# Kernel tuning notes

Measured on AMD Instinct MI355X. Metric: run time of the kernel, lower is better.

The kernel has to match this reference:

```python
import jax, jax.numpy as jnp
import numpy as np

B, M, N, K = 256, 512, 256, 16


def setup_inputs() -> dict:
    key = jax.random.key(0)
    k1, k2, k3, k4 = jax.random.split(key, 4)
    x = jax.random.normal(k1, (B, M, N), dtype=jnp.float32)
    # Linear(in_features=N, out_features=1): weight [1, N], bias [1]
    w_weight = jax.random.normal(k2, (1, N), dtype=jnp.float32) * (2.0 / (N + 1)) ** 0.5
    w_bias = jnp.zeros((1,), dtype=jnp.float32)
    # v: [N, K], xavier_normal
    v = jax.random.normal(k3, (N, K), dtype=jnp.float32) * (2.0 / (N + K)) ** 0.5
    return {"x": x, "w_weight": w_weight, "w_bias": w_bias, "v": v}


def reference(x, w_weight, w_bias, v):
    # Linear term: [B, M, 1]
    l = x @ w_weight.T + w_bias  # broadcasts bias [1]
    # Pairwise interaction. Original: result[b,a,c] = x[b,a] @ (V V^T) @ x[b,c]
    # p[b,a] = 0.5 * (sum_c result[b,a,c] - result[b,a,a])
    # Efficient O(B*M*K) identity: with xv = x @ V,
    #   sum_c result[b,a,c] = xv[b,a] . sum_c xv[b,c]
    #   result[b,a,a]       = ||xv[b,a]||^2
    xv = jnp.einsum('bmn,nk->bmk', x, v)        # [B, M, K]
    sv = xv.sum(axis=1)                          # [B, K]
    row_sum = jnp.einsum('bmk,bk->bm', xv, sv)  # [B, M]
    diag = jnp.sum(xv * xv, axis=-1)             # [B, M]
    p = 0.5 * (row_sum - diag)                   # [B, M]
    return l + p[..., None]                      # [B, M, 1]
```

## Files before the change

### kernel.cpp

```cpp
#include <hip/hip_runtime.h>

#define B_ 256
#define M_ 512
#define N_ 256
#define K_ 16
#define TR 64
#define NT 4

typedef __attribute__((ext_vector_type(8))) short short8;
typedef __attribute__((ext_vector_type(4))) float f32x4;

__device__ __forceinline__ unsigned short f2bf(float f) {
    unsigned u = __builtin_bit_cast(unsigned, f);
    u += 0x7FFFu + ((u >> 16) & 1u);
    return (unsigned short)(u >> 16);
}
__device__ __forceinline__ float bf2f(unsigned short h) {
    unsigned u = ((unsigned)h) << 16;
    return __builtin_bit_cast(float, u);
}

__global__ __launch_bounds__(256) void fm_pass1(
    const float* __restrict__ x, const float* __restrict__ w,
    const float* __restrict__ bias, const float* __restrict__ v,
    float* __restrict__ xv, float* __restrict__ svpart, float* __restrict__ out)
{
    __shared__ __align__(16) unsigned char xL[2][TR * 512];
    __shared__ __align__(16) unsigned short wLb[N_];
    __shared__ __align__(16) float red[64];

    const int t   = threadIdx.x;
    const int l   = t & 63;
    const int wv  = t >> 6;
    const int blk = blockIdx.x;
    const int b   = blk >> 1;
    const int m0  = (blk & 1) * (NT * TR);
    const float bias0 = bias[0];

    if (t < 64) {
        float4 wq = *(const float4*)(w + t * 4);
        wLb[t * 4 + 0] = f2bf(wq.x); wLb[t * 4 + 1] = f2bf(wq.y);
        wLb[t * 4 + 2] = f2bf(wq.z); wLb[t * 4 + 3] = f2bf(wq.w);
    }

    short8 vB[8];
    #pragma unroll
    for (int c = 0; c < 8; ++c) {
        #pragma unroll
        for (int j = 0; j < 8; ++j) {
            float f = v[(size_t)(c * 32 + (l >> 4) * 8 + j) * K_ + (l & 15)];
            vB[c][j] = (short)f2bf(f);
        }
    }

    const float* gx = x + (size_t)(b * M_ + m0) * N_;

    const int swq = l >> 1;
    const int shf = (l & 1) * 8;

    float4 st[16];
    #pragma unroll
    for (int j = 0; j < 16; ++j)
        st[j] = *(const float4*)(gx + j * 1024 + t * 4);
    #pragma unroll
    for (int j = 0; j < 16; ++j) {
        const int row = j * 4 + wv;
        unsigned lo = (unsigned)f2bf(st[j].x) | ((unsigned)f2bf(st[j].y) << 16);
        unsigned hi = (unsigned)f2bf(st[j].z) | ((unsigned)f2bf(st[j].w) << 16);
        unsigned* d = (unsigned*)(xL[0] + row * 512 + ((swq ^ (row & 7)) << 4) + shf);
        d[0] = lo; d[1] = hi;
    }
    __syncthreads();

    f32x4 acc[NT];
    #pragma unroll
    for (int T = 0; T < NT; ++T) acc[T] = f32x4{0.f, 0.f, 0.f, 0.f};

    #pragma unroll
    for (int T = 0; T < NT; ++T) {
        const int cur = T & 1;
        if (T + 1 < NT) {
            #pragma unroll
            for (int j = 0; j < 16; ++j)
                st[j] = *(const float4*)(gx + (size_t)(T + 1) * TR * N_ + j * 1024 + t * 4);
        }

        const int arow = wv * 16 + (l & 15);
        const unsigned char* abase = xL[cur] + arow * 512;
        #pragma unroll
        for (int c = 0; c < 8; ++c) {
            short8 a = *(const short8*)(abase + (((c * 4 + (l >> 4)) ^ (arow & 7)) << 4));
            acc[T] = __builtin_amdgcn_mfma_f32_16x16x32_bf16(a, vB[c], acc[T], 0, 0, 0);
        }

        {
            const int row = t >> 2;
            const int qt  = t & 3;
            const unsigned char* rbase = xL[cur] + row * 512;
            float ls = 0.f;
            #pragma unroll
            for (int i = 0; i < 8; ++i) {
                short8 xs = *(const short8*)(rbase + ((((qt * 8 + i)) ^ (row & 7)) << 4));
                short8 ws = *(const short8*)((const unsigned char*)wLb + qt * 128 + i * 16);
                #pragma unroll
                for (int e = 0; e < 8; ++e)
                    ls += bf2f((unsigned short)xs[e]) * bf2f((unsigned short)ws[e]);
            }
            ls += __shfl_xor(ls, 1);
            ls += __shfl_xor(ls, 2);
            if (qt == 0)
                out[(size_t)b * M_ + m0 + T * TR + row] = ls + bias0;
        }

        if (T + 1 < NT) {
            #pragma unroll
            for (int j = 0; j < 16; ++j) {
                const int row = j * 4 + wv;
                unsigned lo = (unsigned)f2bf(st[j].x) | ((unsigned)f2bf(st[j].y) << 16);
                unsigned hi = (unsigned)f2bf(st[j].z) | ((unsigned)f2bf(st[j].w) << 16);
                unsigned* d = (unsigned*)(xL[cur ^ 1] + row * 512 + ((swq ^ (row & 7)) << 4) + shf);
                d[0] = lo; d[1] = hi;
            }
        }
        __syncthreads();
    }

    #pragma unroll
    for (int T = 0; T < NT; ++T) {
        const int rbase = m0 + T * TR + wv * 16 + (l >> 4) * 4;
        #pragma unroll
        for (int r = 0; r < 4; ++r)
            xv[(size_t)(b * M_ + rbase + r) * K_ + (l & 15)] = acc[T][r];
    }

    float s = 0.f;
    #pragma unroll
    for (int T = 0; T < NT; ++T)
        s += acc[T][0] + acc[T][1] + acc[T][2] + acc[T][3];
    s += __shfl_xor(s, 16);
    s += __shfl_xor(s, 32);
    if (l < 16) red[wv * 16 + l] = s;
    __syncthreads();
    if (t < 16)
        svpart[(size_t)blk * 16 + t] = red[t] + red[16 + t] + red[32 + t] + red[48 + t];
}

__global__ __launch_bounds__(256) void fm_pass2(
    const float* __restrict__ xv, const float* __restrict__ svpart,
    float* __restrict__ out)
{
    const int t = threadIdx.x;
    const int blk = blockIdx.x;
    const int b = blk >> 1;
    const int m = (blk & 1) * 256 + t;
    __shared__ __align__(16) float svL[16];
    if (t < 16)
        svL[t] = svpart[(size_t)(b * 2 + 0) * 16 + t] + svpart[(size_t)(b * 2 + 1) * 16 + t];
    __syncthreads();

    const float4* xvp = (const float4*)(xv + ((size_t)b * M_ + m) * K_);
    float4 a0 = xvp[0], a1 = xvp[1], a2 = xvp[2], a3 = xvp[3];
    const float4* s4 = (const float4*)svL;
    float4 s0 = s4[0], s1 = s4[1], s2 = s4[2], s3 = s4[3];

    float rs = a0.x * s0.x + a0.y * s0.y + a0.z * s0.z + a0.w * s0.w
             + a1.x * s1.x + a1.y * s1.y + a1.z * s1.z + a1.w * s1.w
             + a2.x * s2.x + a2.y * s2.y + a2.z * s2.z + a2.w * s2.w
             + a3.x * s3.x + a3.y * s3.y + a3.z * s3.z + a3.w * s3.w;
    float dg = a0.x * a0.x + a0.y * a0.y + a0.z * a0.z + a0.w * a0.w
             + a1.x * a1.x + a1.y * a1.y + a1.z * a1.z + a1.w * a1.w
             + a2.x * a2.x + a2.y * a2.y + a2.z * a2.z + a2.w * a2.w
             + a3.x * a3.x + a3.y * a3.y + a3.z * a3.z + a3.w * a3.w;

    const size_t o = (size_t)b * M_ + m;
    out[o] = out[o] + 0.5f * (rs - dg);
}

extern "C" void kernel_launch(void* const* d_in, const int* in_sizes, int n_in,
                              void* d_out, int out_size, void* d_ws, size_t ws_size,
                              hipStream_t stream) {
    const float* x    = (const float*)d_in[0];
    const float* w    = (const float*)d_in[1];
    const float* bias = (const float*)d_in[2];
    const float* v    = (const float*)d_in[3];
    float* out = (float*)d_out;

    float* xv     = (float*)d_ws;
    float* svpart = xv + (size_t)B_ * M_ * K_;

    fm_pass1<<<dim3(B_ * 2), dim3(256), 0, stream>>>(x, w, bias, v, xv, svpart, out);
    fm_pass2<<<dim3(B_ * 2), dim3(256), 0, stream>>>(xv, svpart, out);
}
```

Measured before the change: 30.56 us.

## Fuse both FM passes into one kernel with one block per batch

Merges the two kernels into one. Each 512-thread block now handles a whole batch of 512 rows, and the 8 waves split the N reduction in half, combining partial MFMA accumulators through shared memory. The xv intermediate and the svpart round trip through global memory go away, along with the second launch. The trade-off is half as many blocks (256 instead of 512) on a GPU with many CUs, so parallelism drops, and the final stage needs cross-lane shuffles done by only half the waves.

```diff
diff --git a/kernel.cpp b/kernel.cpp
--- a/kernel.cpp
+++ b/kernel.cpp
@@ -5,7 +5,7 @@
 #define N_ 256
 #define K_ 16
 #define TR 64
-#define NT 4
+#define NT 8
 
 typedef __attribute__((ext_vector_type(8))) short short8;
 typedef __attribute__((ext_vector_type(4))) float f32x4;
@@ -20,21 +20,23 @@
     return __builtin_bit_cast(float, u);
 }
 
-__global__ __launch_bounds__(256) void fm_pass1(
+__global__ __launch_bounds__(512) void fm_fused(
     const float* __restrict__ x, const float* __restrict__ w,
     const float* __restrict__ bias, const float* __restrict__ v,
-    float* __restrict__ xv, float* __restrict__ svpart, float* __restrict__ out)
+    float* __restrict__ out)
 {
     __shared__ __align__(16) unsigned char xL[2][TR * 512];
     __shared__ __align__(16) unsigned short wLb[N_];
+    __shared__ __align__(16) float lin[M_];
     __shared__ __align__(16) float red[64];
+    __shared__ __align__(16) float svL[16];
 
     const int t   = threadIdx.x;
     const int l   = t & 63;
     const int wv  = t >> 6;
-    const int blk = blockIdx.x;
-    const int b   = blk >> 1;
-    const int m0  = (blk & 1) * (NT * TR);
+    const int wr  = wv & 3;
+    const int wn  = wv >> 2;
+    const int b   = blockIdx.x;
     const float bias0 = bias[0];
 
     if (t < 64) {
@@ -43,28 +45,28 @@
         wLb[t * 4 + 2] = f2bf(wq.z); wLb[t * 4 + 3] = f2bf(wq.w);
     }
 
-    short8 vB[8];
+    short8 vB[4];
     #pragma unroll
-    for (int c = 0; c < 8; ++c) {
+    for (int c = 0; c < 4; ++c) {
         #pragma unroll
         for (int j = 0; j < 8; ++j) {
-            float f = v[(size_t)(c * 32 + (l >> 4) * 8 + j) * K_ + (l & 15)];
+            float f = v[(size_t)((wn * 4 + c) * 32 + (l >> 4) * 8 + j) * K_ + (l & 15)];
             vB[c][j] = (short)f2bf(f);
         }
     }
 
-    const float* gx = x + (size_t)(b * M_ + m0) * N_;
+    const float* gx = x + (size_t)b * M_ * N_;
 
     const int swq = l >> 1;
     const int shf = (l & 1) * 8;
 
-    float4 st[16];
+    float4 st[8];
     #pragma unroll
-    for (int j = 0; j < 16; ++j)
-        st[j] = *(const float4*)(gx + j * 1024 + t * 4);
+    for (int j = 0; j < 8; ++j)
+        st[j] = *(const float4*)(gx + j * 2048 + t * 4);
     #pragma unroll
-    for (int j = 0; j < 16; ++j) {
-        const int row = j * 4 + wv;
+    for (int j = 0; j < 8; ++j) {
+        const int row = j * 8 + wv;
         unsigned lo = (unsigned)f2bf(st[j].x) | ((unsigned)f2bf(st[j].y) << 16);
         unsigned hi = (unsigned)f2bf(st[j].z) | ((unsigned)f2bf(st[j].w) << 16);
         unsigned* d = (unsigned*)(xL[0] + row * 512 + ((swq ^ (row & 7)) << 4) + shf);
@@ -81,41 +83,43 @@
         const int cur = T & 1;
         if (T + 1 < NT) {
             #pragma unroll
-            for (int j = 0; j < 16; ++j)
-                st[j] = *(const float4*)(gx + (size_t)(T + 1) * TR * N_ + j * 1024 + t * 4);
+            for (int j = 0; j < 8; ++j)
+                st[j] = *(const float4*)(gx + (size_t)(T + 1) * TR * N_ + j * 2048 + t * 4);
         }
 
-        const int arow = wv * 16 + (l & 15);
+        const int arow = wr * 16 + (l & 15);
         const unsigned char* abase = xL[cur] + arow * 512;
         #pragma unroll
-        for (int c = 0; c < 8; ++c) {
-            short8 a = *(const short8*)(abase + (((c * 4 + (l >> 4)) ^ (arow & 7)) << 4));
+        for (int c = 0; c < 4; ++c) {
+            const int cq = (wn * 4 + c) * 4 + (l >> 4);
+            short8 a = *(const short8*)(abase + ((cq ^ (arow & 7)) << 4));
             acc[T] = __builtin_amdgcn_mfma_f32_16x16x32_bf16(a, vB[c], acc[T], 0, 0, 0);
         }
 
         {
-            const int row = t >> 2;
-            const int qt  = t & 3;
+            const int row = t >> 3;
+            const int qt  = t & 7;
             const unsigned char* rbase = xL[cur] + row * 512;
             float ls = 0.f;
             #pragma unroll
-            for (int i = 0; i < 8; ++i) {
-                short8 xs = *(const short8*)(rbase + ((((qt * 8 + i)) ^ (row & 7)) << 4));
-                short8 ws = *(const short8*)((const unsigned char*)wLb + qt * 128 + i * 16);
+            for (int i = 0; i < 4; ++i) {
+                const int qi = qt * 4 + i;
+                short8 xs = *(const short8*)(rbase + ((qi ^ (row & 7)) << 4));
+                short8 ws = *(const short8*)((const unsigned char*)wLb + qi * 16);
                 #pragma unroll
                 for (int e = 0; e < 8; ++e)
                     ls += bf2f((unsigned short)xs[e]) * bf2f((unsigned short)ws[e]);
             }
             ls += __shfl_xor(ls, 1);
             ls += __shfl_xor(ls, 2);
-            if (qt == 0)
-                out[(size_t)b * M_ + m0 + T * TR + row] = ls + bias0;
+            ls += __shfl_xor(ls, 4);
+            if (qt == 0) lin[T * TR + row] = ls;
         }
 
         if (T + 1 < NT) {
             #pragma unroll
-            for (int j = 0; j < 16; ++j) {
-                const int row = j * 4 + wv;
+            for (int j = 0; j < 8; ++j) {
+                const int row = j * 8 + wv;
                 unsigned lo = (unsigned)f2bf(st[j].x) | ((unsigned)f2bf(st[j].y) << 16);
                 unsigned hi = (unsigned)f2bf(st[j].z) | ((unsigned)f2bf(st[j].w) << 16);
                 unsigned* d = (unsigned*)(xL[cur ^ 1] + row * 512 + ((swq ^ (row & 7)) << 4) + shf);
@@ -125,55 +129,55 @@
         __syncthreads();
     }
 
-    #pragma unroll
-    for (int T = 0; T < NT; ++T) {
-        const int rbase = m0 + T * TR + wv * 16 + (l >> 4) * 4;
+    float* exch = (float*)xL[0];
+    const int pos = (wr * 64 + l) * 32;
+    if (wn == 1) {
         #pragma unroll
-        for (int r = 0; r < 4; ++r)
-            xv[(size_t)(b * M_ + rbase + r) * K_ + (l & 15)] = acc[T][r];
+        for (int T = 0; T < NT; ++T)
+            *(f32x4*)(exch + pos + T * 4) = acc[T];
+    }
+    __syncthreads();
+    if (wn == 0) {
+        #pragma unroll
+        for (int T = 0; T < NT; ++T) {
+            f32x4 o = *(const f32x4*)(exch + pos + T * 4);
+            acc[T][0] += o[0]; acc[T][1] += o[1];
+            acc[T][2] += o[2]; acc[T][3] += o[3];
+        }
     }
 
     float s = 0.f;
-    #pragma unroll
-    for (int T = 0; T < NT; ++T)
-        s += acc[T][0] + acc[T][1] + acc[T][2] + acc[T][3];
+    if (wn == 0) {
+        #pragma unroll
+        for (int T = 0; T < NT; ++T)
+            s += acc[T][0] + acc[T][1] + acc[T][2] + acc[T][3];
+    }
     s += __shfl_xor(s, 16);
     s += __shfl_xor(s, 32);
-    if (l < 16) red[wv * 16 + l] = s;
+    if (wn == 0 && l < 16) red[wr * 16 + l] = s;
     __syncthreads();
-    if (t < 16)
-        svpart[(size_t)blk * 16 + t] = red[t] + red[16 + t] + red[32 + t] + red[48 + t];
-}
-
-__global__ __launch_bounds__(256) void fm_pass2(
-    const float* __restrict__ xv, const float* __restrict__ svpart,
-    float* __restrict__ out)
-{
-    const int t = threadIdx.x;
-    const int blk = blockIdx.x;
-    const int b = blk >> 1;
-    const int m = (blk & 1) * 256 + t;
-    __shared__ __align__(16) float svL[16];
-    if (t < 16)
-        svL[t] = svpart[(size_t)(b * 2 + 0) * 16 + t] + svpart[(size_t)(b * 2 + 1) * 16 + t];
+    if (t < 16) svL[t] = red[t] + red[16 + t] + red[32 + t] + red[48 + t];
     __syncthreads();
 
-    const float4* xvp = (const float4*)(xv + ((size_t)b * M_ + m) * K_);
-    float4 a0 = xvp[0], a1 = xvp[1], a2 = xvp[2], a3 = xvp[3];
-    const float4* s4 = (const float4*)svL;
-    float4 s0 = s4[0], s1 = s4[1], s2 = s4[2], s3 = s4[3];
-
-    float rs = a0.x * s0.x + a0.y * s0.y + a0.z * s0.z + a0.w * s0.w
-             + a1.x * s1.x + a1.y * s1.y + a1.z * s1.z + a1.w * s1.w
-             + a2.x * s2.x + a2.y * s2.y + a2.z * s2.z + a2.w * s2.w
-             + a3.x * s3.x + a3.y * s3.y + a3.z * s3.z + a3.w * s3.w;
-    float dg = a0.x * a0.x + a0.y * a0.y + a0.z * a0.z + a0.w * a0.w
-             + a1.x * a1.x + a1.y * a1.y + a1.z * a1.z + a1.w * a1.w
-             + a2.x * a2.x + a2.y * a2.y + a2.z * a2.z + a2.w * a2.w
-             + a3.x * a3.x + a3.y * a3.y + a3.z * a3.z + a3.w * a3.w;
-
-    const size_t o = (size_t)b * M_ + m;
-    out[o] = out[o] + 0.5f * (rs - dg);
+    if (wn == 0) {
+        const float svk = svL[l & 15];
+        #pragma unroll
+        for (int T = 0; T < NT; ++T) {
+            #pragma unroll
+            for (int r = 0; r < 4; ++r) {
+                const float a = acc[T][r];
+                float q = a * (svk - a);
+                q += __shfl_xor(q, 1);
+                q += __shfl_xor(q, 2);
+                q += __shfl_xor(q, 4);
+                q += __shfl_xor(q, 8);
+                if ((l & 15) == 0) {
+                    const int row = T * TR + wr * 16 + (l >> 4) * 4 + r;
+                    out[(size_t)b * M_ + row] = lin[row] + bias0 + 0.5f * q;
+                }
+            }
+        }
+    }
 }
 
 extern "C" void kernel_launch(void* const* d_in, const int* in_sizes, int n_in,
@@ -185,9 +189,5 @@
     const float* v    = (const float*)d_in[3];
     float* out = (float*)d_out;
 
-    float* xv     = (float*)d_ws;
-    float* svpart = xv + (size_t)B_ * M_ * K_;
-
-    fm_pass1<<<dim3(B_ * 2), dim3(256), 0, stream>>>(x, w, bias, v, xv, svpart, out);
-    fm_pass2<<<dim3(B_ * 2), dim3(256), 0, stream>>>(xv, svpart, out);
+    fm_fused<<<dim3(B_), dim3(512), 0, stream>>>(x, w, bias, v, out);
 }
```

Measured after the change: 31.47 us. 1.03x slower.

## Fuse two passes into one kernel with sibling-block flag handshake

Applied to the files above, without the earlier changes.

Merges the two kernels into one. Each block keeps its xv tile in registers instead of writing it to global memory, and exchanges its partial column sum with its sibling block through an atomic release/acquire flag. This removes the xv round trip through memory and the second launch. In exchange it adds a hipMemsetAsync per call, and the spin-wait on the sibling block risks deadlock if the two sibling blocks are not co-resident. That is unlikely with 512 blocks on this GPU.

```diff
diff --git a/kernel.cpp b/kernel.cpp
--- a/kernel.cpp
+++ b/kernel.cpp
@@ -6,6 +6,7 @@
 #define K_ 16
 #define TR 64
 #define NT 4
+#define NBLK (B_ * 2)
 
 typedef __attribute__((ext_vector_type(8))) short short8;
 typedef __attribute__((ext_vector_type(4))) float f32x4;
@@ -20,14 +21,17 @@
     return __builtin_bit_cast(float, u);
 }
 
-__global__ __launch_bounds__(256) void fm_pass1(
+__global__ __launch_bounds__(256) void fm_fused(
     const float* __restrict__ x, const float* __restrict__ w,
     const float* __restrict__ bias, const float* __restrict__ v,
-    float* __restrict__ xv, float* __restrict__ svpart, float* __restrict__ out)
+    float* __restrict__ svpart, int* __restrict__ flags,
+    float* __restrict__ out)
 {
     __shared__ __align__(16) unsigned char xL[2][TR * 512];
     __shared__ __align__(16) unsigned short wLb[N_];
+    __shared__ __align__(16) float lin[NT * TR];
     __shared__ __align__(16) float red[64];
+    __shared__ __align__(16) float svO[16];
 
     const int t   = threadIdx.x;
     const int l   = t & 63;
@@ -35,6 +39,7 @@
     const int blk = blockIdx.x;
     const int b   = blk >> 1;
     const int m0  = (blk & 1) * (NT * TR);
+    const int sib = blk ^ 1;
     const float bias0 = bias[0];
 
     if (t < 64) {
@@ -108,8 +113,7 @@
             }
             ls += __shfl_xor(ls, 1);
             ls += __shfl_xor(ls, 2);
-            if (qt == 0)
-                out[(size_t)b * M_ + m0 + T * TR + row] = ls + bias0;
+            if (qt == 0) lin[T * TR + row] = ls;
         }
 
         if (T + 1 < NT) {
@@ -125,14 +129,6 @@
         __syncthreads();
     }
 
-    #pragma unroll
-    for (int T = 0; T < NT; ++T) {
-        const int rbase = m0 + T * TR + wv * 16 + (l >> 4) * 4;
-        #pragma unroll
-        for (int r = 0; r < 4; ++r)
-            xv[(size_t)(b * M_ + rbase + r) * K_ + (l & 15)] = acc[T][r];
-    }
-
     float s = 0.f;
     #pragma unroll
     for (int T = 0; T < NT; ++T)
@@ -141,39 +137,43 @@
     s += __shfl_xor(s, 32);
     if (l < 16) red[wv * 16 + l] = s;
     __syncthreads();
-    if (t < 16)
-        svpart[(size_t)blk * 16 + t] = red[t] + red[16 + t] + red[32 + t] + red[48 + t];
-}
-
-__global__ __launch_bounds__(256) void fm_pass2(
-    const float* __restrict__ xv, const float* __restrict__ svpart,
-    float* __restrict__ out)
-{
-    const int t = threadIdx.x;
-    const int blk = blockIdx.x;
-    const int b = blk >> 1;
-    const int m = (blk & 1) * 256 + t;
-    __shared__ __align__(16) float svL[16];
-    if (t < 16)
-        svL[t] = svpart[(size_t)(b * 2 + 0) * 16 + t] + svpart[(size_t)(b * 2 + 1) * 16 + t];
+    if (t < 16) {
+        const float p = red[t] + red[16 + t] + red[32 + t] + red[48 + t];
+        svO[t] = p;
+        __hip_atomic_store(svpart + (size_t)blk * 16 + t, p,
+                           __ATOMIC_RELEASE, __HIP_MEMORY_SCOPE_AGENT);
+    }
     __syncthreads();
 
-    const float4* xvp = (const float4*)(xv + ((size_t)b * M_ + m) * K_);
-    float4 a0 = xvp[0], a1 = xvp[1], a2 = xvp[2], a3 = xvp[3];
-    const float4* s4 = (const float4*)svL;
-    float4 s0 = s4[0], s1 = s4[1], s2 = s4[2], s3 = s4[3];
+    if (t == 0) {
+        __threadfence();
+        __hip_atomic_store(flags + blk, 1, __ATOMIC_RELEASE, __HIP_MEMORY_SCOPE_AGENT);
+        while (__hip_atomic_load(flags + sib, __ATOMIC_ACQUIRE,
+                                 __HIP_MEMORY_SCOPE_AGENT) == 0)
+            __builtin_amdgcn_s_sleep(1);
+    }
+    __syncthreads();
 
-    float rs = a0.x * s0.x + a0.y * s0.y + a0.z * s0.z + a0.w * s0.w
-             + a1.x * s1.x + a1.y * s1.y + a1.z * s1.z + a1.w * s1.w
-             + a2.x * s2.x + a2.y * s2.y + a2.z * s2.z + a2.w * s2.w
-             + a3.x * s3.x + a3.y * s3.y + a3.z * s3.z + a3.w * s3.w;
-    float dg = a0.x * a0.x + a0.y * a0.y + a0.z * a0.z + a0.w * a0.w
-             + a1.x * a1.x + a1.y * a1.y + a1.z * a1.z + a1.w * a1.w
-             + a2.x * a2.x + a2.y * a2.y + a2.z * a2.z + a2.w * a2.w
-             + a3.x * a3.x + a3.y * a3.y + a3.z * a3.z + a3.w * a3.w;
+    const float svk = svO[l & 15] +
+        __hip_atomic_load(svpart + (size_t)sib * 16 + (l & 15),
+                          __ATOMIC_RELAXED, __HIP_MEMORY_SCOPE_AGENT);
 
-    const size_t o = (size_t)b * M_ + m;
-    out[o] = out[o] + 0.5f * (rs - dg);
+    #pragma unroll
+    for (int T = 0; T < NT; ++T) {
+        #pragma unroll
+        for (int r = 0; r < 4; ++r) {
+            const float a = acc[T][r];
+            float q = a * (svk - a);
+            q += __shfl_xor(q, 1);
+            q += __shfl_xor(q, 2);
+            q += __shfl_xor(q, 4);
+            q += __shfl_xor(q, 8);
+            if ((l & 15) == 0) {
+                const int row = T * TR + wv * 16 + (l >> 4) * 4 + r;
+                out[(size_t)b * M_ + m0 + row] = lin[row] + bias0 + 0.5f * q;
+            }
+        }
+    }
 }
 
 extern "C" void kernel_launch(void* const* d_in, const int* in_sizes, int n_in,
@@ -185,9 +185,9 @@
     const float* v    = (const float*)d_in[3];
     float* out = (float*)d_out;
 
-    float* xv     = (float*)d_ws;
-    float* svpart = xv + (size_t)B_ * M_ * K_;
+    float* svpart = (float*)d_ws;
+    int*   flags  = (int*)((char*)d_ws + (64 << 10));
 
-    fm_pass1<<<dim3(B_ * 2), dim3(256), 0, stream>>>(x, w, bias, v, xv, svpart, out);
-    fm_pass2<<<dim3(B_ * 2), dim3(256), 0, stream>>>(xv, svpart, out);
+    hipMemsetAsync(flags, 0, NBLK * sizeof(int), stream);
+    fm_fused<<<dim3(NBLK), dim3(256), 0, stream>>>(x, w, bias, v, svpart, flags, out);
 }
```

Result: slower. 76.97 us (+151.9%).
